# Kernel optimization log

Measured on AMD Instinct MI355X. Metric: run time of the kernel, lower is better.

The kernel has to match this reference:

```python
import jax, jax.numpy as jnp
import numpy as np

B, N, D = 16, 2048, 64

def setup_inputs() -> dict:
    key = jax.random.key(0)
    kq, kk, kv = jax.random.split(key, 3)
    q = jax.random.normal(kq, (B, N, D), dtype=jnp.float32)
    k = jax.random.normal(kk, (B, N, D), dtype=jnp.float32)
    v = jax.random.normal(kv, (B, N, D), dtype=jnp.float32)
    return {"q": q, "k": k, "v": v}

def reference(q, k, v):
    d_k = q.shape[-1]
    # scores: [B, N, N] = q @ k^T, scaled by 1/sqrt(d_k) (applied after matmul, as in source)
    scores = jnp.einsum('bnd,bmd->bnm', q, k)
    attn = jax.nn.softmax(scores / np.sqrt(d_k).astype(q.dtype), axis=-1)
    out = jnp.einsum('bnm,bmd->bnd', attn, v)
    return out
```

## Files before the change

### kernel.cpp

```cpp
#include <hip/hip_runtime.h>

#define B_  16
#define N_  2048
#define D_  64
#define QB  128
#define KB  64
#define NT  (N_/KB)
#define NW  8
#define TILE_ELEMS (KB * D_)

typedef __attribute__((ext_vector_type(8))) short short8;
typedef __attribute__((ext_vector_type(4))) float f32x4;
typedef unsigned short u16_t;

static __device__ __forceinline__ unsigned cvt_pk_bf16(float lo, float hi) {
  unsigned r;
  asm("v_cvt_pk_bf16_f32 %0, %1, %2" : "=v"(r) : "v"(lo), "v"(hi));
  return r;
}
static __device__ __forceinline__ float exp2_fast(float x) {
  float r;
  asm("v_exp_f32 %0, %1" : "=v"(r) : "v"(x));
  return r;
}
static __device__ __forceinline__ void gload_lds16(const void* g, void* l) {
  __builtin_amdgcn_global_load_lds(
      (const __attribute__((address_space(1))) unsigned*)g,
      (__attribute__((address_space(3))) unsigned*)l, 16, 0, 0);
}

union U8 { unsigned u[4]; short8 s8; };

__global__ __launch_bounds__(256) void prep_kernel(
    const float* __restrict__ kg, const float* __restrict__ vg,
    u16_t* __restrict__ kimg, u16_t* __restrict__ vimg) {
  const int bid = blockIdx.x;
  const int isV = bid & 1;
  const int tileid = bid >> 1;
  const float* src = (isV ? vg : kg) + (size_t)tileid * TILE_ELEMS;
  u16_t* dst = (isV ? vimg : kimg) + (size_t)tileid * TILE_ELEMS;
  const int tid = threadIdx.x;

  if (!isV) {
#pragma unroll
    for (int p = 0; p < 2; ++p) {
      int c = tid + p * 256;
      int row = c >> 3, c8 = c & 7;
      const float* sp = src + row * 64 + c8 * 8;
      float4 f0 = *(const float4*)sp;
      float4 f1 = *(const float4*)(sp + 4);
      uint4 u;
      u.x = cvt_pk_bf16(f0.x, f0.y);
      u.y = cvt_pk_bf16(f0.z, f0.w);
      u.z = cvt_pk_bf16(f1.x, f1.y);
      u.w = cvt_pk_bf16(f1.z, f1.w);
      *(uint4*)&dst[(row * 64 + c8 * 8) ^ ((row & 7) << 3)] = u;
    }
  } else {
    __shared__ float Vl[64][68];
    int row = tid >> 2, q4 = (tid & 3) * 16;
    const float* sp = src + row * 64 + q4;
#pragma unroll
    for (int i = 0; i < 4; ++i)
      *(float4*)&Vl[row][q4 + i * 4] = *(const float4*)(sp + i * 4);
    __syncthreads();
#pragma unroll
    for (int p = 0; p < 2; ++p) {
      int c = tid + p * 256;
      int d = c >> 3, kc = c & 7;
      float x[8];
#pragma unroll
      for (int j = 0; j < 8; ++j) x[j] = Vl[kc * 8 + j][d];
      uint4 u;
      u.x = cvt_pk_bf16(x[0], x[1]);
      u.y = cvt_pk_bf16(x[2], x[3]);
      u.z = cvt_pk_bf16(x[4], x[5]);
      u.w = cvt_pk_bf16(x[6], x[7]);
      *(uint4*)&dst[(d * 64 + kc * 8) ^ ((d & 7) << 3)] = u;
    }
  }
}

__global__ __launch_bounds__(512, 2) void attn_main(
    const float* __restrict__ qg, const u16_t* __restrict__ kimg,
    const u16_t* __restrict__ vimg, float* __restrict__ outg) {
  __shared__ __align__(16) u16_t Kl[2][TILE_ELEMS];
  __shared__ __align__(16) u16_t Vt[2][TILE_ELEMS];
  __shared__ __align__(16) u16_t Pl[NW][16 * KB];

  const int tid = threadIdx.x;
  const int w = tid >> 6, l = tid & 63;
  const int g = l >> 4, qi = l & 15;
  const int bidx = blockIdx.x;
  const int logical = (bidx & 7) * 32 + (bidx >> 3);
  const int b = logical >> 4, qt = logical & 15;
  const int q0 = qt * QB + w * 16;

  short8 qf[2];
  {
    const float s = 0.18033688011112042f;
    const float* qp = qg + ((size_t)(b * N_ + q0 + qi)) * D_;
#pragma unroll
    for (int dc = 0; dc < 2; ++dc) {
      float4 f0 = *(const float4*)(qp + dc * 32 + g * 8);
      float4 f1 = *(const float4*)(qp + dc * 32 + g * 8 + 4);
      U8 u;
      u.u[0] = cvt_pk_bf16(f0.x * s, f0.y * s);
      u.u[1] = cvt_pk_bf16(f0.z * s, f0.w * s);
      u.u[2] = cvt_pk_bf16(f1.x * s, f1.y * s);
      u.u[3] = cvt_pk_bf16(f1.z * s, f1.w * s);
      qf[dc] = u.s8;
    }
  }

  f32x4 acc[4] = {{0,0,0,0},{0,0,0,0},{0,0,0,0},{0,0,0,0}};
  float m_run = -INFINITY;
  float l_run = 0.f;

  const u16_t* kt = kimg + (size_t)b * NT * TILE_ELEMS;
  const u16_t* vt = vimg + (size_t)b * NT * TILE_ELEMS;

  auto stage = [&](int bb, int tt) {
    const u16_t* kp = kt + (size_t)tt * TILE_ELEMS + w * 512 + l * 8;
    const u16_t* vp = vt + (size_t)tt * TILE_ELEMS + w * 512 + l * 8;
    gload_lds16(kp, &Kl[bb][w * 512]);
    gload_lds16(vp, &Vt[bb][w * 512]);
  };

  stage(0, 0);
  __syncthreads();

  for (int t = 0; t < NT; ++t) {
    const int cur = t & 1;
    if (t + 1 < NT) stage(cur ^ 1, t + 1);
    const u16_t* Kc = Kl[cur];
    const u16_t* Vc = Vt[cur];

    f32x4 st[4];
    __builtin_amdgcn_s_setprio(1);
#pragma unroll
    for (int kvt = 0; kvt < 4; ++kvt) {
      int kvr = kvt * 16 + qi;
      int base = kvr * 64, sw = (kvr & 7) << 3;
      short8 kf0 = *(const short8*)&Kc[(base + g * 8) ^ sw];
      short8 kf1 = *(const short8*)&Kc[(base + 32 + g * 8) ^ sw];
      f32x4 z = {0, 0, 0, 0};
      z = __builtin_amdgcn_mfma_f32_16x16x32_bf16(kf0, qf[0], z, 0, 0, 0);
      z = __builtin_amdgcn_mfma_f32_16x16x32_bf16(kf1, qf[1], z, 0, 0, 0);
      st[kvt] = z;
    }
    __builtin_amdgcn_s_setprio(0);

    float m01 = fmaxf(fmaxf(st[0][0], st[0][1]), fmaxf(st[0][2], st[0][3]));
    float m23 = fmaxf(fmaxf(st[1][0], st[1][1]), fmaxf(st[1][2], st[1][3]));
    float m45 = fmaxf(fmaxf(st[2][0], st[2][1]), fmaxf(st[2][2], st[2][3]));
    float m67 = fmaxf(fmaxf(st[3][0], st[3][1]), fmaxf(st[3][2], st[3][3]));
    float mloc = fmaxf(fmaxf(m01, m23), fmaxf(m45, m67));
    mloc = fmaxf(mloc, __shfl_xor(mloc, 16));
    mloc = fmaxf(mloc, __shfl_xor(mloc, 32));
    if (__any(mloc > m_run + 8.0f)) {
      float mnew = fmaxf(m_run, mloc);
      float alpha = exp2_fast(m_run - mnew);
      m_run = mnew;
      l_run *= alpha;
#pragma unroll
      for (int dt = 0; dt < 4; ++dt)
#pragma unroll
        for (int r = 0; r < 4; ++r) acc[dt][r] *= alpha;
    }
    float ps = 0.f;
#pragma unroll
    for (int kvt = 0; kvt < 4; ++kvt)
#pragma unroll
      for (int r = 0; r < 4; ++r) {
        float p = exp2_fast(st[kvt][r] - m_run);
        st[kvt][r] = p;
        ps += p;
      }
    ps += __shfl_xor(ps, 16);
    ps += __shfl_xor(ps, 32);
    l_run += ps;

#pragma unroll
    for (int kvt = 0; kvt < 4; ++kvt) {
      unsigned u0 = cvt_pk_bf16(st[kvt][0], st[kvt][1]);
      unsigned u1 = cvt_pk_bf16(st[kvt][2], st[kvt][3]);
      int kv = kvt * 16 + g * 4;
      int sw = (qi & 7) << 3;
      *(unsigned*)&Pl[w][(qi * 64 + kv) ^ sw]     = u0;
      *(unsigned*)&Pl[w][(qi * 64 + kv + 2) ^ sw] = u1;
    }
    asm volatile("s_waitcnt lgkmcnt(0)" ::: "memory");

    __builtin_amdgcn_s_setprio(1);
#pragma unroll
    for (int kk = 0; kk < 2; ++kk) {
      short8 pf = *(const short8*)&Pl[w][(qi * 64 + kk * 32 + g * 8) ^ ((qi & 7) << 3)];
#pragma unroll
      for (int dt = 0; dt < 4; ++dt) {
        int d = dt * 16 + qi;
        short8 vf = *(const short8*)&Vc[(d * 64 + kk * 32 + g * 8) ^ ((d & 7) << 3)];
        acc[dt] = __builtin_amdgcn_mfma_f32_16x16x32_bf16(vf, pf, acc[dt], 0, 0, 0);
      }
    }
    __builtin_amdgcn_s_setprio(0);
    __syncthreads();
  }

  float rl = 1.0f / l_run;
  float* op = outg + ((size_t)(b * N_ + q0 + qi)) * D_;
#pragma unroll
  for (int dt = 0; dt < 4; ++dt) {
    float4 o;
    o.x = acc[dt][0] * rl;
    o.y = acc[dt][1] * rl;
    o.z = acc[dt][2] * rl;
    o.w = acc[dt][3] * rl;
    *(float4*)(op + dt * 16 + g * 4) = o;
  }
}

__global__ __launch_bounds__(512, 2) void attn_fwd_fallback(
    const float* __restrict__ qg, const float* __restrict__ kg,
    const float* __restrict__ vg, float* __restrict__ outg) {
  __shared__ __align__(16) u16_t Kl[KB * D_];
  __shared__ __align__(16) u16_t Vt[D_ * KB];
  __shared__ __align__(16) u16_t Pl[NW][16 * KB];

  const int tid = threadIdx.x;
  const int w = tid >> 6, l = tid & 63;
  const int g = l >> 4, qi = l & 15;
  const int bidx = blockIdx.x;
  const int b = bidx >> 4, qt = bidx & 15;
  const int q0 = qt * QB + w * 16;

  short8 qf[2];
  {
    const float* qp = qg + ((size_t)(b * N_ + q0 + qi)) * D_;
    const float s = 0.125f;
#pragma unroll
    for (int dc = 0; dc < 2; ++dc) {
      float4 f0 = *(const float4*)(qp + dc * 32 + g * 8);
      float4 f1 = *(const float4*)(qp + dc * 32 + g * 8 + 4);
      U8 u;
      u.u[0] = cvt_pk_bf16(f0.x * s, f0.y * s);
      u.u[1] = cvt_pk_bf16(f0.z * s, f0.w * s);
      u.u[2] = cvt_pk_bf16(f1.x * s, f1.y * s);
      u.u[3] = cvt_pk_bf16(f1.z * s, f1.w * s);
      qf[dc] = u.s8;
    }
  }

  f32x4 acc[4] = {{0,0,0,0},{0,0,0,0},{0,0,0,0},{0,0,0,0}};
  float m_run = -INFINITY, l_run = 0.f;
  const float* kbase = kg + (size_t)b * N_ * D_;
  const float* vbase = vg + (size_t)b * N_ * D_;

  for (int kv0 = 0; kv0 < N_; kv0 += KB) {
#pragma unroll
    for (int p = 0; p < 2; ++p) {
      int idx = tid + p * 512;
      int row = idx >> 4, c4 = idx & 15;
      float4 f = *(const float4*)(kbase + (size_t)(kv0 + row) * D_ + c4 * 4);
      unsigned u0 = cvt_pk_bf16(f.x, f.y);
      unsigned u1 = cvt_pk_bf16(f.z, f.w);
      int o = (row * 64 + c4 * 4) ^ ((row & 7) << 3);
      *(uint2*)&Kl[o] = make_uint2(u0, u1);
    }
    {
      int rp = tid >> 4, c4 = tid & 15;
      int row2 = rp * 2;
      const float* vp = vbase + (size_t)(kv0 + row2) * D_ + c4 * 4;
      float4 a0 = *(const float4*)vp;
      float4 a1 = *(const float4*)(vp + D_);
      float lo[4] = {a0.x, a0.y, a0.z, a0.w};
      float hi[4] = {a1.x, a1.y, a1.z, a1.w};
#pragma unroll
      for (int i = 0; i < 4; ++i) {
        int d = c4 * 4 + i;
        unsigned u = cvt_pk_bf16(lo[i], hi[i]);
        int o = (d * 64 + row2) ^ ((d & 7) << 3);
        *(unsigned*)&Vt[o] = u;
      }
    }
    __syncthreads();

    f32x4 st[4];
#pragma unroll
    for (int kvt = 0; kvt < 4; ++kvt) {
      int kvr = kvt * 16 + qi;
      int base = kvr * 64, sw = (kvr & 7) << 3;
      short8 kf0 = *(const short8*)&Kl[(base + g * 8) ^ sw];
      short8 kf1 = *(const short8*)&Kl[(base + 32 + g * 8) ^ sw];
      f32x4 z = {0, 0, 0, 0};
      z = __builtin_amdgcn_mfma_f32_16x16x32_bf16(kf0, qf[0], z, 0, 0, 0);
      z = __builtin_amdgcn_mfma_f32_16x16x32_bf16(kf1, qf[1], z, 0, 0, 0);
      st[kvt] = z;
    }

    float mloc = -INFINITY;
#pragma unroll
    for (int kvt = 0; kvt < 4; ++kvt)
#pragma unroll
      for (int r = 0; r < 4; ++r) mloc = fmaxf(mloc, st[kvt][r]);
    mloc = fmaxf(mloc, __shfl_xor(mloc, 16));
    mloc = fmaxf(mloc, __shfl_xor(mloc, 32));
    float mnew = fmaxf(m_run, mloc);
    float alpha = __expf(m_run - mnew);
    m_run = mnew;

    float ps = 0.f;
#pragma unroll
    for (int kvt = 0; kvt < 4; ++kvt)
#pragma unroll
      for (int r = 0; r < 4; ++r) {
        float p = __expf(st[kvt][r] - mnew);
        st[kvt][r] = p;
        ps += p;
      }
    ps += __shfl_xor(ps, 16);
    ps += __shfl_xor(ps, 32);
    l_run = l_run * alpha + ps;

#pragma unroll
    for (int dt = 0; dt < 4; ++dt)
#pragma unroll
      for (int r = 0; r < 4; ++r) acc[dt][r] *= alpha;

#pragma unroll
    for (int kvt = 0; kvt < 4; ++kvt) {
      unsigned u0 = cvt_pk_bf16(st[kvt][0], st[kvt][1]);
      unsigned u1 = cvt_pk_bf16(st[kvt][2], st[kvt][3]);
      int kv = kvt * 16 + g * 4;
      int sw = (qi & 7) << 3;
      *(unsigned*)&Pl[w][(qi * 64 + kv) ^ sw]     = u0;
      *(unsigned*)&Pl[w][(qi * 64 + kv + 2) ^ sw] = u1;
    }
    asm volatile("s_waitcnt lgkmcnt(0)" ::: "memory");

#pragma unroll
    for (int kk = 0; kk < 2; ++kk) {
      short8 pf = *(const short8*)&Pl[w][(qi * 64 + kk * 32 + g * 8) ^ ((qi & 7) << 3)];
#pragma unroll
      for (int dt = 0; dt < 4; ++dt) {
        int d = dt * 16 + qi;
        short8 vf = *(const short8*)&Vt[(d * 64 + kk * 32 + g * 8) ^ ((d & 7) << 3)];
        acc[dt] = __builtin_amdgcn_mfma_f32_16x16x32_bf16(vf, pf, acc[dt], 0, 0, 0);
      }
    }
    __syncthreads();
  }

  float rl = 1.0f / l_run;
  float* op = outg + ((size_t)(b * N_ + q0 + qi)) * D_;
#pragma unroll
  for (int dt = 0; dt < 4; ++dt) {
    float4 o;
    o.x = acc[dt][0] * rl;
    o.y = acc[dt][1] * rl;
    o.z = acc[dt][2] * rl;
    o.w = acc[dt][3] * rl;
    *(float4*)(op + dt * 16 + g * 4) = o;
  }
}

extern "C" void kernel_launch(void* const* d_in, const int* in_sizes, int n_in,
                              void* d_out, int out_size, void* d_ws, size_t ws_size,
                              hipStream_t stream) {
  const float* q = (const float*)d_in[0];
  const float* k = (const float*)d_in[1];
  const float* v = (const float*)d_in[2];
  float* out = (float*)d_out;

  const size_t img_elems = (size_t)B_ * N_ * D_;
  const size_t need = 2 * img_elems * sizeof(u16_t);

  if (ws_size >= need) {
    u16_t* kimg = (u16_t*)d_ws;
    u16_t* vimg = kimg + img_elems;
    prep_kernel<<<dim3(B_ * NT * 2), dim3(256), 0, stream>>>(k, v, kimg, vimg);
    attn_main<<<dim3(B_ * (N_ / QB)), dim3(512), 0, stream>>>(q, kimg, vimg, out);
  } else {
    attn_fwd_fallback<<<dim3(B_ * (N_ / QB)), dim3(512), 0, stream>>>(q, k, v, out);
  }
}
```

Measured before the change: 117.8 us.

## Split KV dimension across blocks with a separate combine kernel

Partitions the key/value sequence into four splits, so each query tile is processed by four blocks that each write unnormalized partial accumulators plus running max and sum to workspace. A new combine kernel merges the partials with log-sum-exp weighting. This raises the grid from 256 blocks to 1024 to fill more of the GPU's compute units, and the launch bounds are raised to allow more resident blocks. The cost is extra workspace traffic and an additional kernel launch. It only takes effect when the workspace is large enough.

```diff
diff --git a/kernel.cpp b/kernel.cpp
--- a/kernel.cpp
+++ b/kernel.cpp
@@ -81,9 +81,12 @@
   }
 }
 
-__global__ __launch_bounds__(512, 2) void attn_main(
+template <int SPLIT>
+__global__ __launch_bounds__(512, 6) void attn_main(
     const float* __restrict__ qg, const u16_t* __restrict__ kimg,
-    const u16_t* __restrict__ vimg, float* __restrict__ outg) {
+    const u16_t* __restrict__ vimg, float* __restrict__ outg,
+    float* __restrict__ pacc, float* __restrict__ pml) {
+  constexpr int TS = NT / SPLIT;
   __shared__ __align__(16) u16_t Kl[2][TILE_ELEMS];
   __shared__ __align__(16) u16_t Vt[2][TILE_ELEMS];
   __shared__ __align__(16) u16_t Pl[NW][16 * KB];
@@ -91,24 +94,28 @@
   const int tid = threadIdx.x;
   const int w = tid >> 6, l = tid & 63;
   const int g = l >> 4, qi = l & 15;
+
+  constexpr int TOT = B_ * 16 * SPLIT;
   const int bidx = blockIdx.x;
-  const int logical = (bidx & 7) * 32 + (bidx >> 3);
-  const int b = logical >> 4, qt = logical & 15;
+  const int logical = (bidx & 7) * (TOT / 8) + (bidx >> 3);
+  const int s  = logical & (SPLIT - 1);
+  const int qt = (logical / SPLIT) & 15;
+  const int b  = logical / (SPLIT * 16);
   const int q0 = qt * QB + w * 16;
 
   short8 qf[2];
   {
-    const float s = 0.18033688011112042f;
+    const float sc = 0.18033688011112042f;
     const float* qp = qg + ((size_t)(b * N_ + q0 + qi)) * D_;
 #pragma unroll
     for (int dc = 0; dc < 2; ++dc) {
       float4 f0 = *(const float4*)(qp + dc * 32 + g * 8);
       float4 f1 = *(const float4*)(qp + dc * 32 + g * 8 + 4);
       U8 u;
-      u.u[0] = cvt_pk_bf16(f0.x * s, f0.y * s);
-      u.u[1] = cvt_pk_bf16(f0.z * s, f0.w * s);
-      u.u[2] = cvt_pk_bf16(f1.x * s, f1.y * s);
-      u.u[3] = cvt_pk_bf16(f1.z * s, f1.w * s);
+      u.u[0] = cvt_pk_bf16(f0.x * sc, f0.y * sc);
+      u.u[1] = cvt_pk_bf16(f0.z * sc, f0.w * sc);
+      u.u[2] = cvt_pk_bf16(f1.x * sc, f1.y * sc);
+      u.u[3] = cvt_pk_bf16(f1.z * sc, f1.w * sc);
       qf[dc] = u.s8;
     }
   }
@@ -127,12 +134,13 @@
     gload_lds16(vp, &Vt[bb][w * 512]);
   };
 
-  stage(0, 0);
+  const int t0 = s * TS;
+  stage(0, t0);
   __syncthreads();
 
-  for (int t = 0; t < NT; ++t) {
-    const int cur = t & 1;
-    if (t + 1 < NT) stage(cur ^ 1, t + 1);
+  for (int i = 0; i < TS; ++i) {
+    const int cur = i & 1;
+    if (i + 1 < TS) stage(cur ^ 1, t0 + i + 1);
     const u16_t* Kc = Kl[cur];
     const u16_t* Vc = Vt[cur];
 
@@ -207,17 +215,71 @@
     __syncthreads();
   }
 
-  float rl = 1.0f / l_run;
-  float* op = outg + ((size_t)(b * N_ + q0 + qi)) * D_;
-#pragma unroll
-  for (int dt = 0; dt < 4; ++dt) {
-    float4 o;
-    o.x = acc[dt][0] * rl;
-    o.y = acc[dt][1] * rl;
-    o.z = acc[dt][2] * rl;
-    o.w = acc[dt][3] * rl;
-    *(float4*)(op + dt * 16 + g * 4) = o;
-  }
+  const int wq = w * 16 + qi;
+  if constexpr (SPLIT == 1) {
+    float rl = 1.0f / l_run;
+    float* op = outg + ((size_t)(b * N_ + qt * QB + wq)) * D_;
+#pragma unroll
+    for (int dt = 0; dt < 4; ++dt) {
+      float4 o;
+      o.x = acc[dt][0] * rl;
+      o.y = acc[dt][1] * rl;
+      o.z = acc[dt][2] * rl;
+      o.w = acc[dt][3] * rl;
+      *(float4*)(op + dt * 16 + g * 4) = o;
+    }
+  } else {
+    const size_t rowid = (size_t)logical * QB + wq;
+    float* ap = pacc + rowid * D_;
+#pragma unroll
+    for (int dt = 0; dt < 4; ++dt) {
+      float4 o;
+      o.x = acc[dt][0]; o.y = acc[dt][1]; o.z = acc[dt][2]; o.w = acc[dt][3];
+      *(float4*)(ap + dt * 16 + g * 4) = o;
+    }
+    if (g == 0) *(float2*)&pml[rowid * 2] = make_float2(m_run, l_run);
+  }
+}
+
+template <int SPLIT>
+__global__ __launch_bounds__(256) void combine_kernel(
+    const float* __restrict__ pacc, const float* __restrict__ pml,
+    float* __restrict__ outg) {
+  const int fid = blockIdx.x * 256 + threadIdx.x;
+  const int q = fid >> 4;
+  const int c = fid & 15;
+  const int b = q >> 11, rem = q & 2047;
+  const int qt = rem >> 7, wq = rem & 127;
+  const size_t base = ((size_t)(b * 16 + qt) * SPLIT) * QB + wq;
+
+  float m[SPLIT], lv[SPLIT];
+#pragma unroll
+  for (int s2 = 0; s2 < SPLIT; ++s2) {
+    float2 ml = *(const float2*)&pml[(base + (size_t)s2 * QB) * 2];
+    m[s2] = ml.x; lv[s2] = ml.y;
+  }
+  float ms = m[0];
+#pragma unroll
+  for (int s2 = 1; s2 < SPLIT; ++s2) ms = fmaxf(ms, m[s2]);
+  float L = 0.f, wgt[SPLIT];
+#pragma unroll
+  for (int s2 = 0; s2 < SPLIT; ++s2) {
+    wgt[s2] = exp2_fast(m[s2] - ms);
+    L += wgt[s2] * lv[s2];
+  }
+  float rl = 1.0f / L;
+
+  float4 o = {0.f, 0.f, 0.f, 0.f};
+#pragma unroll
+  for (int s2 = 0; s2 < SPLIT; ++s2) {
+    float4 a = *(const float4*)&pacc[(base + (size_t)s2 * QB) * D_ + c * 4];
+    o.x += wgt[s2] * a.x;
+    o.y += wgt[s2] * a.y;
+    o.z += wgt[s2] * a.z;
+    o.w += wgt[s2] * a.w;
+  }
+  o.x *= rl; o.y *= rl; o.z *= rl; o.w *= rl;
+  *(float4*)&outg[(size_t)fid * 4] = o;
 }
 
 __global__ __launch_bounds__(512, 2) void attn_fwd_fallback(
@@ -237,16 +299,16 @@
   short8 qf[2];
   {
     const float* qp = qg + ((size_t)(b * N_ + q0 + qi)) * D_;
-    const float s = 0.125f;
+    const float sc = 0.125f;
 #pragma unroll
     for (int dc = 0; dc < 2; ++dc) {
       float4 f0 = *(const float4*)(qp + dc * 32 + g * 8);
       float4 f1 = *(const float4*)(qp + dc * 32 + g * 8 + 4);
       U8 u;
-      u.u[0] = cvt_pk_bf16(f0.x * s, f0.y * s);
-      u.u[1] = cvt_pk_bf16(f0.z * s, f0.w * s);
-      u.u[2] = cvt_pk_bf16(f1.x * s, f1.y * s);
-      u.u[3] = cvt_pk_bf16(f1.z * s, f1.w * s);
+      u.u[0] = cvt_pk_bf16(f0.x * sc, f0.y * sc);
+      u.u[1] = cvt_pk_bf16(f0.z * sc, f0.w * sc);
+      u.u[2] = cvt_pk_bf16(f1.x * sc, f1.y * sc);
+      u.u[3] = cvt_pk_bf16(f1.z * sc, f1.w * sc);
       qf[dc] = u.s8;
     }
   }
@@ -372,15 +434,31 @@
   const float* v = (const float*)d_in[2];
   float* out = (float*)d_out;
 
+  constexpr int SPLIT = 4;
   const size_t img_elems = (size_t)B_ * N_ * D_;
-  const size_t need = 2 * img_elems * sizeof(u16_t);
-
-  if (ws_size >= need) {
+  const size_t img_bytes = 2 * img_elems * sizeof(u16_t);
+  const size_t rows = (size_t)B_ * N_ * SPLIT;
+  const size_t acc_bytes = rows * D_ * sizeof(float);
+  const size_t ml_bytes = rows * 2 * sizeof(float);
+  const size_t need_split = img_bytes + acc_bytes + ml_bytes;
+
+  if (ws_size >= need_split) {
+    u16_t* kimg = (u16_t*)d_ws;
+    u16_t* vimg = kimg + img_elems;
+    float* pacc = (float*)((char*)d_ws + img_bytes);
+    float* pml  = pacc + rows * D_;
+    prep_kernel<<<dim3(B_ * NT * 2), dim3(256), 0, stream>>>(k, v, kimg, vimg);
+    attn_main<SPLIT><<<dim3(B_ * 16 * SPLIT), dim3(512), 0, stream>>>(
+        q, kimg, vimg, out, pacc, pml);
+    combine_kernel<SPLIT><<<dim3((B_ * N_ * D_ / 4) / 256), dim3(256), 0, stream>>>(
+        pacc, pml, out);
+  } else if (ws_size >= img_bytes) {
     u16_t* kimg = (u16_t*)d_ws;
     u16_t* vimg = kimg + img_elems;
     prep_kernel<<<dim3(B_ * NT * 2), dim3(256), 0, stream>>>(k, v, kimg, vimg);
-    attn_main<<<dim3(B_ * (N_ / QB)), dim3(512), 0, stream>>>(q, kimg, vimg, out);
+    attn_main<1><<<dim3(B_ * 16), dim3(512), 0, stream>>>(
+        q, kimg, vimg, out, nullptr, nullptr);
   } else {
-    attn_fwd_fallback<<<dim3(B_ * (N_ / QB)), dim3(512), 0, stream>>>(q, k, v, out);
-  }
-}
+    attn_fwd_fallback<<<dim3(B_ * 16), dim3(512), 0, stream>>>(q, k, v, out);
+  }
+}
```

Result: faster. 112.4 us (median of 2 runs) (-4.6%).
